# Kernel tuning notes

Measured on AMD Instinct MI355X. Metric: run time of the kernel, lower is better.

## Reference

```python
import jax, jax.numpy as jnp
import numpy as np

EPS = 1e-5

def setup_inputs() -> dict:
    key = jax.random.key(0)
    ks = jax.random.split(key, 10)
    B, S, C, Q, D = 16, 2048, 768, 1024, 64
    clamp3_features = jax.random.normal(ks[0], (B, S, C), dtype=jnp.float32)
    residual = jax.random.normal(ks[1], (B, S, Q), dtype=jnp.float32)
    # params (xavier-ish scale; up-proj given small random values instead of zeros
    # so the output is non-trivial for correctness testing)
    Wproj = jax.random.normal(ks[2], (Q, C), dtype=jnp.float32) * (1.0 / np.sqrt(C))
    Wdown = jax.random.normal(ks[3], (D, Q), dtype=jnp.float32) * (1.0 / np.sqrt(Q))
    gamma = jnp.ones((D,), dtype=jnp.float32)
    beta = jnp.zeros((D,), dtype=jnp.float32)
    Wl1 = jax.random.normal(ks[4], (D, D), dtype=jnp.float32) * (1.0 / np.sqrt(D))
    bl1 = jnp.zeros((D,), dtype=jnp.float32)
    Wl2 = jax.random.normal(ks[5], (D, D), dtype=jnp.float32) * (1.0 / np.sqrt(D))
    bl2 = jnp.zeros((D,), dtype=jnp.float32)
    Wup = jax.random.normal(ks[6], (Q, D), dtype=jnp.float32) * (1.0 / np.sqrt(D))
    return {"clamp3_features": clamp3_features, "residual": residual,
            "Wproj": Wproj, "Wdown": Wdown, "gamma": gamma, "beta": beta,
            "Wl1": Wl1, "bl1": bl1, "Wl2": Wl2, "bl2": bl2, "Wup": Wup}

def _layernorm(x, gamma, beta):
    mu = jnp.mean(x, axis=-1, keepdims=True)
    var = jnp.mean(jnp.square(x - mu), axis=-1, keepdims=True)
    return (x - mu) * jax.lax.rsqrt(var + EPS) * gamma + beta

def reference(clamp3_features, residual, Wproj, Wdown, gamma, beta, Wl1, bl1, Wl2, bl2, Wup):
    # projection (no bias) -> down (no bias) -> LayerNorm
    projected = jnp.einsum('bsc,qc->bsq', clamp3_features, Wproj)
    down = jnp.einsum('bsq,dq->bsd', projected, Wdown)
    normed = _layernorm(down, gamma, beta)
    # SwiGLU: swish(l1(x)) * l2(x)
    o1 = jnp.einsum('bsd,ed->bse', normed, Wl1) + bl1
    swish = o1 * jax.nn.sigmoid(o1)
    gate = jnp.einsum('bsd,ed->bse', normed, Wl2) + bl2
    activated = swish * gate  # dropout is identity in eval mode
    up = jnp.einsum('bsd,qd->bsq', activated, Wup)
    return residual + up
```

## Files before the change

kernel.cpp:

```cpp
#include <hip/hip_runtime.h>


#define CDIM 768
#define QDIM 1024

typedef __attribute__((ext_vector_type(8))) short bf16x8;
typedef __attribute__((ext_vector_type(4))) float f32x4;

__device__ __forceinline__ ushort f2bf(float f) {
  union { float f; unsigned u; } v; v.f = f;
  unsigned r = v.u + 0x7fffu + ((v.u >> 16) & 1u);
  return (ushort)(r >> 16);
}

__global__ void k_wcomb(const float* __restrict__ Wproj, const float* __restrict__ Wdown,
                        float* __restrict__ part) {
  int bid = blockIdx.x;
  int cb = bid % 12, db = (bid / 12) % 8, qc = bid / 96;
  int l = threadIdx.x;
  int c = cb * 64 + l;
  float acc[8];
  #pragma unroll
  for (int i = 0; i < 8; ++i) acc[i] = 0.f;
  int q0 = qc * 128;
  for (int q = q0; q < q0 + 128; ++q) {
    float xp = Wproj[q * CDIM + c];
    #pragma unroll
    for (int i = 0; i < 8; ++i)
      acc[i] = fmaf(Wdown[(db * 8 + i) * QDIM + q], xp, acc[i]);
  }
  #pragma unroll
  for (int i = 0; i < 8; ++i)
    part[((size_t)qc * CDIM + c) * 64 + db * 8 + i] = acc[i];
}

__global__ void k_arrange(const float* __restrict__ part, const float* __restrict__ Wup,
                          const float* __restrict__ Wl1, const float* __restrict__ Wl2,
                          ushort* __restrict__ wcf, ushort* __restrict__ wupf,
                          ushort* __restrict__ wl1f, ushort* __restrict__ wl2f) {
  int idx = blockIdx.x * 256 + threadIdx.x;
  if (idx < 49152) {
    int i0 = idx;
    int j = i0 & 7, l = (i0 >> 3) & 63, t = i0 >> 9;
    int g = l >> 4, r16 = l & 15;
    int nf = t & 3, ks = t >> 2;
    int k = 32 * ks + 8 * g + j, n = 16 * nf + r16;
    float s = 0.f;
    #pragma unroll
    for (int qc = 0; qc < 8; ++qc) s += part[((size_t)qc * CDIM + k) * 64 + n];
    wcf[i0] = f2bf(s);
  } else if (idx < 49152 + 65536) {
    int i2 = idx - 49152;
    int j = i2 & 7, l = (i2 >> 3) & 63, t = i2 >> 9;
    int g = l >> 4, r16 = l & 15;
    int ks = t & 1, nf = t >> 1;
    int k = 32 * ks + 8 * g + j, n = 16 * nf + r16;
    wupf[i2] = f2bf(Wup[n * 64 + k]);
  } else if (idx < 49152 + 65536 + 4096) {
    int i3 = idx - (49152 + 65536);
    int j = i3 & 7, l = (i3 >> 3) & 63, t = i3 >> 9;
    int g = l >> 4, r16 = l & 15;
    int nf = t & 3, ks = t >> 2;
    int k = 32 * ks + 8 * g + j, e = 16 * nf + r16;
    wl1f[i3] = f2bf(Wl1[e * 64 + k]);
  } else {
    int i4 = idx - (49152 + 65536 + 4096);
    int j = i4 & 7, l = (i4 >> 3) & 63, t = i4 >> 9;
    int g = l >> 4, r16 = l & 15;
    int nf = t & 3, ks = t >> 2;
    int k = 32 * ks + 8 * g + j, e = 16 * nf + r16;
    wl2f[i4] = f2bf(Wl2[e * 64 + k]);
  }
}

__global__ __launch_bounds__(256, 6)
void k_act(const float* __restrict__ xg,
           const float* __restrict__ gamma, const float* __restrict__ beta,
           const float* __restrict__ bl1, const float* __restrict__ bl2,
           const ushort* __restrict__ wcf,
           const ushort* __restrict__ wl1f, const ushort* __restrict__ wl2f,
           ushort* __restrict__ ag) {
  __shared__ ushort smem[12416];
  ushort (*x_lds)[776] = reinterpret_cast<ushort(*)[776]>(smem);
  float  (*d_lds)[68]  = reinterpret_cast<float (*)[68]>(smem);
  ushort (*n_lds)[72]  = reinterpret_cast<ushort(*)[72]>(reinterpret_cast<char*>(smem) + 4608);
  ushort (*a_lds)[72]  = reinterpret_cast<ushort(*)[72]>(reinterpret_cast<char*>(smem) + 8192);

  const int tid = threadIdx.x;
  const int w = tid >> 6, l = tid & 63, g = l >> 4, r16 = l & 15;
  const int row0 = blockIdx.x * 16;

  #pragma unroll
  for (int i = 0; i < 12; ++i) {
    int f4 = i * 256 + tid;
    int r = f4 / 192;
    int c4 = (f4 - r * 192) * 4;
    const float4 v = *reinterpret_cast<const float4*>(xg + (size_t)(row0 + r) * CDIM + c4);
    ushort4 b;
    b.x = f2bf(v.x); b.y = f2bf(v.y); b.z = f2bf(v.z); b.w = f2bf(v.w);
    *reinterpret_cast<ushort4*>(&x_lds[r][c4]) = b;
  }
  __syncthreads();

  f32x4 dacc = {0.f, 0.f, 0.f, 0.f};
  #pragma unroll 8
  for (int ks = 0; ks < 24; ++ks) {
    bf16x8 a = *reinterpret_cast<const bf16x8*>(&x_lds[r16][ks * 32 + 8 * g]);
    bf16x8 b = *reinterpret_cast<const bf16x8*>(wcf + ((size_t)(ks * 4 + w) * 64 + l) * 8);
    dacc = __builtin_amdgcn_mfma_f32_16x16x32_bf16(a, b, dacc, 0, 0, 0);
  }
  __syncthreads();
  #pragma unroll
  for (int rg = 0; rg < 4; ++rg) d_lds[4 * g + rg][16 * w + r16] = dacc[rg];
  __syncthreads();

  {
    int row = 4 * w + g;
    f32x4 v = *reinterpret_cast<const f32x4*>(&d_lds[row][4 * r16]);
    float s  = v[0] + v[1] + v[2] + v[3];
    float sq = v[0]*v[0] + v[1]*v[1] + v[2]*v[2] + v[3]*v[3];
    #pragma unroll
    for (int m = 1; m < 16; m <<= 1) {
      s  += __shfl_xor(s, m, 64);
      sq += __shfl_xor(sq, m, 64);
    }
    float mu  = s * (1.f / 64.f);
    float var = sq * (1.f / 64.f) - mu * mu;
    float rs  = rsqrtf(var + 1e-5f);
    const float4 gm = *reinterpret_cast<const float4*>(gamma + 4 * r16);
    const float4 bt = *reinterpret_cast<const float4*>(beta  + 4 * r16);
    ushort4 nb;
    nb.x = f2bf((v[0] - mu) * rs * gm.x + bt.x);
    nb.y = f2bf((v[1] - mu) * rs * gm.y + bt.y);
    nb.z = f2bf((v[2] - mu) * rs * gm.z + bt.z);
    nb.w = f2bf((v[3] - mu) * rs * gm.w + bt.w);
    *reinterpret_cast<ushort4*>(&n_lds[row][4 * r16]) = nb;
  }
  __syncthreads();

  {
    bf16x8 a0 = *reinterpret_cast<const bf16x8*>(&n_lds[r16][8 * g]);
    bf16x8 a1 = *reinterpret_cast<const bf16x8*>(&n_lds[r16][32 + 8 * g]);
    bf16x8 b10 = *reinterpret_cast<const bf16x8*>(wl1f + ((size_t)(0 * 4 + w) * 64 + l) * 8);
    bf16x8 b11 = *reinterpret_cast<const bf16x8*>(wl1f + ((size_t)(1 * 4 + w) * 64 + l) * 8);
    bf16x8 b20 = *reinterpret_cast<const bf16x8*>(wl2f + ((size_t)(0 * 4 + w) * 64 + l) * 8);
    bf16x8 b21 = *reinterpret_cast<const bf16x8*>(wl2f + ((size_t)(1 * 4 + w) * 64 + l) * 8);
    f32x4 z = {0.f, 0.f, 0.f, 0.f};
    f32x4 acc1 = __builtin_amdgcn_mfma_f32_16x16x32_bf16(a0, b10, z, 0, 0, 0);
    acc1 = __builtin_amdgcn_mfma_f32_16x16x32_bf16(a1, b11, acc1, 0, 0, 0);
    f32x4 acc2 = __builtin_amdgcn_mfma_f32_16x16x32_bf16(a0, b20, z, 0, 0, 0);
    acc2 = __builtin_amdgcn_mfma_f32_16x16x32_bf16(a1, b21, acc2, 0, 0, 0);
    float bv1 = bl1[16 * w + r16];
    float bv2 = bl2[16 * w + r16];
    #pragma unroll
    for (int rg = 0; rg < 4; ++rg) {
      float o1 = acc1[rg] + bv1;
      float o2 = acc2[rg] + bv2;
      float sw = o1 / (1.f + __expf(-o1));
      a_lds[4 * g + rg][16 * w + r16] = f2bf(sw * o2);
    }
  }
  __syncthreads();

  if (tid < 128) {
    int r = tid >> 3, c = 8 * (tid & 7);
    bf16x8 v = *reinterpret_cast<const bf16x8*>(&a_lds[r][c]);
    *reinterpret_cast<bf16x8*>(ag + (size_t)(row0 + r) * 64 + c) = v;
  }
}

__global__ __launch_bounds__(256, 3)
void k_up(const ushort* __restrict__ ag, const float* __restrict__ resg,
          const ushort* __restrict__ wupf, float* __restrict__ outg) {
  __shared__ float  bounce[16][512];
  __shared__ ushort a_lds[16][68];
  const int tid = threadIdx.x;
  const int w = tid >> 6, l = tid & 63, g = l >> 4, r16 = l & 15;
  const int row0 = blockIdx.x * 16;

  {
    int e = tid * 4;
    int r = e >> 6, c = e & 63;
    ushort4 v = *reinterpret_cast<const ushort4*>(ag + (size_t)(row0 + r) * 64 + c);
    *reinterpret_cast<ushort4*>(&a_lds[r][c]) = v;
  }
  __syncthreads();
  const bf16x8 af0 = *reinterpret_cast<const bf16x8*>(&a_lds[r16][8 * g]);
  const bf16x8 af1 = *reinterpret_cast<const bf16x8*>(&a_lds[r16][32 + 8 * g]);

  #pragma unroll
  for (int p = 0; p < 2; ++p) {
    f32x4 acc[8];
    #pragma unroll
    for (int i = 0; i < 8; ++i) {
      size_t nf = 32 * p + 8 * w + i;
      bf16x8 b0 = *reinterpret_cast<const bf16x8*>(wupf + ((nf * 2 + 0) * 64 + l) * 8);
      bf16x8 b1 = *reinterpret_cast<const bf16x8*>(wupf + ((nf * 2 + 1) * 64 + l) * 8);
      f32x4 t = {0.f, 0.f, 0.f, 0.f};
      t = __builtin_amdgcn_mfma_f32_16x16x32_bf16(b0, af0, t, 0, 0, 0);
      acc[i] = __builtin_amdgcn_mfma_f32_16x16x32_bf16(b1, af1, t, 0, 0, 0);
    }
    if (p) __syncthreads();
    #pragma unroll
    for (int i = 0; i < 8; ++i) {
      int q = 32 * w + 4 * i + g;
      *reinterpret_cast<f32x4*>(&bounce[r16][4 * (q ^ (r16 & 7))]) = acc[i];
    }
    __syncthreads();
    #pragma unroll
    for (int s = 0; s < 8; ++s) {
      int row = 2 * s + (tid >> 7);
      int cq  = tid & 127;
      size_t goff = (size_t)(row0 + row) * QDIM + 512 * p + 4 * cq;
      f32x4 rv = *reinterpret_cast<const f32x4*>(resg + goff);
      f32x4 bv = *reinterpret_cast<const f32x4*>(&bounce[row][4 * (cq ^ (row & 7))]);
      *reinterpret_cast<f32x4*>(outg + goff) = rv + bv;
    }
  }
}

extern "C" void kernel_launch(void* const* d_in, const int* in_sizes, int n_in,
                              void* d_out, int out_size, void* d_ws, size_t ws_size,
                              hipStream_t stream) {
  (void)in_sizes; (void)n_in; (void)out_size; (void)ws_size;
  const float* x     = (const float*)d_in[0];
  const float* resid = (const float*)d_in[1];
  const float* Wproj = (const float*)d_in[2];
  const float* Wdown = (const float*)d_in[3];
  const float* gamma = (const float*)d_in[4];
  const float* beta  = (const float*)d_in[5];
  const float* Wl1   = (const float*)d_in[6];
  const float* bl1   = (const float*)d_in[7];
  const float* Wl2   = (const float*)d_in[8];
  const float* bl2   = (const float*)d_in[9];
  const float* Wup   = (const float*)d_in[10];
  float* out = (float*)d_out;

  char* ws = (char*)d_ws;
  float*  part = (float*)(ws);
  ushort* wcf  = (ushort*)(ws + 1572864);
  ushort* wupf = (ushort*)(ws + 1671168);
  ushort* wl1f = (ushort*)(ws + 1802240);
  ushort* wl2f = (ushort*)(ws + 1810432);
  ushort* ag   = (ushort*)(ws + 1818624);

  k_wcomb  <<<768, 64, 0, stream>>>(Wproj, Wdown, part);
  k_arrange<<<480, 256, 0, stream>>>(part, Wup, Wl1, Wl2, wcf, wupf, wl1f, wl2f);
  k_act    <<<2048, 256, 0, stream>>>(x, gamma, beta, bl1, bl2, wcf, wl1f, wl2f, ag);
  k_up     <<<2048, 256, 0, stream>>>(ag, resid, wupf, out);
}
```

Before: 126.1 us.

## Stream activations and residual via async global-to-LDS loads with pipelined ring

k_act now copies fp32 input rows straight into swizzled LDS with global_load_lds and converts to bf16 at fragment-load time, which doubles LDS use and lowers the occupancy hint. k_up computes all 64 output fragments in one pass, stores the up-projection as bf16 in a swizzled bounce buffer, and streams residual rows through a 4-slot LDS ring using async loads with manual vmcnt waits. The aim is to overlap the residual reads with compute and cut register and LDS pressure. The trade-offs are lower occupancy in k_act, and rounding the up-projection to bf16 before the residual add adds precision error.

```diff
diff --git a/kernel.cpp b/kernel.cpp
--- a/kernel.cpp
+++ b/kernel.cpp
@@ -1,4 +1,5 @@
 #include <hip/hip_runtime.h>
+#include <hip/hip_bf16.h>
 
 
 #define CDIM 768
@@ -6,11 +7,20 @@
 
 typedef __attribute__((ext_vector_type(8))) short bf16x8;
 typedef __attribute__((ext_vector_type(4))) float f32x4;
+
+#define WAITV(n) asm volatile("s_waitcnt vmcnt(" #n ")" ::: "memory")
+#define SCHED0() __builtin_amdgcn_sched_barrier(0)
 
 __device__ __forceinline__ ushort f2bf(float f) {
   union { float f; unsigned u; } v; v.f = f;
   unsigned r = v.u + 0x7fffu + ((v.u >> 16) & 1u);
   return (ushort)(r >> 16);
+}
+
+__device__ __forceinline__ void gload16(const float* g, float* lds) {
+  __builtin_amdgcn_global_load_lds(
+      (const __attribute__((address_space(1))) void*)g,
+      (__attribute__((address_space(3))) void*)lds, 16, 0, 0);
 }
 
 __global__ void k_wcomb(const float* __restrict__ Wproj, const float* __restrict__ Wdown,
@@ -73,18 +83,18 @@
   }
 }
 
-__global__ __launch_bounds__(256, 6)
+__global__ __launch_bounds__(256, 3)
 void k_act(const float* __restrict__ xg,
            const float* __restrict__ gamma, const float* __restrict__ beta,
            const float* __restrict__ bl1, const float* __restrict__ bl2,
            const ushort* __restrict__ wcf,
            const ushort* __restrict__ wl1f, const ushort* __restrict__ wl2f,
            ushort* __restrict__ ag) {
-  __shared__ ushort smem[12416];
-  ushort (*x_lds)[776] = reinterpret_cast<ushort(*)[776]>(smem);
+  __shared__ alignas(16) ushort smem[24576];
   float  (*d_lds)[68]  = reinterpret_cast<float (*)[68]>(smem);
   ushort (*n_lds)[72]  = reinterpret_cast<ushort(*)[72]>(reinterpret_cast<char*>(smem) + 4608);
   ushort (*a_lds)[72]  = reinterpret_cast<ushort(*)[72]>(reinterpret_cast<char*>(smem) + 8192);
+  float* xf = reinterpret_cast<float*>(smem);
 
   const int tid = threadIdx.x;
   const int w = tid >> 6, l = tid & 63, g = l >> 4, r16 = l & 15;
@@ -93,21 +103,28 @@
   #pragma unroll
   for (int i = 0; i < 12; ++i) {
     int f4 = i * 256 + tid;
-    int r = f4 / 192;
-    int c4 = (f4 - r * 192) * 4;
-    const float4 v = *reinterpret_cast<const float4*>(xg + (size_t)(row0 + r) * CDIM + c4);
-    ushort4 b;
-    b.x = f2bf(v.x); b.y = f2bf(v.y); b.z = f2bf(v.z); b.w = f2bf(v.w);
-    *reinterpret_cast<ushort4*>(&x_lds[r][c4]) = b;
+    int r  = f4 / 192;
+    int u  = f4 - r * 192;
+    const float* src = xg + (size_t)(row0 + r) * CDIM + ((u ^ (r & 7)) << 2);
+    gload16(src, xf + (size_t)(i * 256 + (w << 6)) * 4);
   }
   __syncthreads();
 
   f32x4 dacc = {0.f, 0.f, 0.f, 0.f};
+  const int rx = r16 & 7;
+  const float* rowp = xf + r16 * 768;
   #pragma unroll 8
   for (int ks = 0; ks < 24; ++ks) {
-    bf16x8 a = *reinterpret_cast<const bf16x8*>(&x_lds[r16][ks * 32 + 8 * g]);
+    int u0 = ks * 8 + 2 * g;
+    f32x4 xa = *reinterpret_cast<const f32x4*>(rowp + ((u0 ^ rx) << 2));
+    f32x4 xb = *reinterpret_cast<const f32x4*>(rowp + (((u0 + 1) ^ rx) << 2));
+    union { bf16x8 v; __hip_bfloat16 h[8]; } fa;
+    fa.h[0] = __float2bfloat16(xa[0]); fa.h[1] = __float2bfloat16(xa[1]);
+    fa.h[2] = __float2bfloat16(xa[2]); fa.h[3] = __float2bfloat16(xa[3]);
+    fa.h[4] = __float2bfloat16(xb[0]); fa.h[5] = __float2bfloat16(xb[1]);
+    fa.h[6] = __float2bfloat16(xb[2]); fa.h[7] = __float2bfloat16(xb[3]);
     bf16x8 b = *reinterpret_cast<const bf16x8*>(wcf + ((size_t)(ks * 4 + w) * 64 + l) * 8);
-    dacc = __builtin_amdgcn_mfma_f32_16x16x32_bf16(a, b, dacc, 0, 0, 0);
+    dacc = __builtin_amdgcn_mfma_f32_16x16x32_bf16(fa.v, b, dacc, 0, 0, 0);
   }
   __syncthreads();
   #pragma unroll
@@ -172,8 +189,9 @@
 __global__ __launch_bounds__(256, 3)
 void k_up(const ushort* __restrict__ ag, const float* __restrict__ resg,
           const ushort* __restrict__ wupf, float* __restrict__ outg) {
-  __shared__ float  bounce[16][512];
-  __shared__ ushort a_lds[16][68];
+  __shared__ alignas(16) ushort a_lds[16][68];
+  __shared__ alignas(16) ushort bounce[16][1024];
+  __shared__ alignas(16) float  ring[4][1024];
   const int tid = threadIdx.x;
   const int w = tid >> 6, l = tid & 63, g = l >> 4, r16 = l & 15;
   const int row0 = blockIdx.x * 16;
@@ -184,38 +202,61 @@
     ushort4 v = *reinterpret_cast<const ushort4*>(ag + (size_t)(row0 + r) * 64 + c);
     *reinterpret_cast<ushort4*>(&a_lds[r][c]) = v;
   }
-  __syncthreads();
-  const bf16x8 af0 = *reinterpret_cast<const bf16x8*>(&a_lds[r16][8 * g]);
-  const bf16x8 af1 = *reinterpret_cast<const bf16x8*>(&a_lds[r16][32 + 8 * g]);
-
-  #pragma unroll
-  for (int p = 0; p < 2; ++p) {
-    f32x4 acc[8];
-    #pragma unroll
-    for (int i = 0; i < 8; ++i) {
-      size_t nf = 32 * p + 8 * w + i;
+  asm volatile("s_waitcnt lgkmcnt(0)" ::: "memory");
+  __builtin_amdgcn_s_barrier();
+  SCHED0();
+
+  #pragma unroll
+  for (int s = 0; s < 3; ++s)
+    gload16(resg + (size_t)(row0 + s) * QDIM + 4 * tid, &ring[s][w << 8]);
+  SCHED0();
+
+  {
+    const bf16x8 af0 = *reinterpret_cast<const bf16x8*>(&a_lds[r16][8 * g]);
+    const bf16x8 af1 = *reinterpret_cast<const bf16x8*>(&a_lds[r16][32 + 8 * g]);
+    #pragma unroll
+    for (int i = 0; i < 16; ++i) {
+      size_t nf = 16 * w + i;
       bf16x8 b0 = *reinterpret_cast<const bf16x8*>(wupf + ((nf * 2 + 0) * 64 + l) * 8);
       bf16x8 b1 = *reinterpret_cast<const bf16x8*>(wupf + ((nf * 2 + 1) * 64 + l) * 8);
       f32x4 t = {0.f, 0.f, 0.f, 0.f};
       t = __builtin_amdgcn_mfma_f32_16x16x32_bf16(b0, af0, t, 0, 0, 0);
-      acc[i] = __builtin_amdgcn_mfma_f32_16x16x32_bf16(b1, af1, t, 0, 0, 0);
+      t = __builtin_amdgcn_mfma_f32_16x16x32_bf16(b1, af1, t, 0, 0, 0);
+      ushort4 ub;
+      ub.x = f2bf(t[0]); ub.y = f2bf(t[1]); ub.z = f2bf(t[2]); ub.w = f2bf(t[3]);
+      int q = 64 * w + 4 * i + g;
+      int p = q ^ ((r16 & 7) << 2);
+      *reinterpret_cast<ushort4*>(&bounce[r16][p << 2]) = ub;
     }
-    if (p) __syncthreads();
-    #pragma unroll
-    for (int i = 0; i < 8; ++i) {
-      int q = 32 * w + 4 * i + g;
-      *reinterpret_cast<f32x4*>(&bounce[r16][4 * (q ^ (r16 & 7))]) = acc[i];
-    }
-    __syncthreads();
-    #pragma unroll
-    for (int s = 0; s < 8; ++s) {
-      int row = 2 * s + (tid >> 7);
-      int cq  = tid & 127;
-      size_t goff = (size_t)(row0 + row) * QDIM + 512 * p + 4 * cq;
-      f32x4 rv = *reinterpret_cast<const f32x4*>(resg + goff);
-      f32x4 bv = *reinterpret_cast<const f32x4*>(&bounce[row][4 * (cq ^ (row & 7))]);
-      *reinterpret_cast<f32x4*>(outg + goff) = rv + bv;
-    }
+  }
+  asm volatile("s_waitcnt lgkmcnt(0)" ::: "memory");
+  __builtin_amdgcn_s_barrier();
+  SCHED0();
+
+  #pragma unroll
+  for (int s = 0; s < 16; ++s) {
+    SCHED0();
+    if (s < 13)
+      gload16(resg + (size_t)(row0 + s + 3) * QDIM + 4 * tid, &ring[(s + 3) & 3][w << 8]);
+    SCHED0();
+    if      (s == 0)  WAITV(3);
+    else if (s == 1)  WAITV(4);
+    else if (s == 2)  WAITV(5);
+    else if (s <= 12) WAITV(6);
+    else if (s == 13) WAITV(5);
+    else if (s == 14) WAITV(4);
+    else              WAITV(3);
+    SCHED0();
+    f32x4 rv = *reinterpret_cast<const f32x4*>(&ring[s & 3][tid << 2]);
+    int p = tid ^ ((s & 7) << 2);
+    ushort4 ub = *reinterpret_cast<const ushort4*>(&bounce[s][p << 2]);
+    union { float f; unsigned u; } c0, c1, c2, c3;
+    c0.u = (unsigned)ub.x << 16; c1.u = (unsigned)ub.y << 16;
+    c2.u = (unsigned)ub.z << 16; c3.u = (unsigned)ub.w << 16;
+    f32x4 o;
+    o[0] = rv[0] + c0.f; o[1] = rv[1] + c1.f;
+    o[2] = rv[2] + c2.f; o[3] = rv[3] + c3.f;
+    *reinterpret_cast<f32x4*>(outg + (size_t)(row0 + s) * QDIM + 4 * tid) = o;
   }
 }
 
```

After: 130.7 us. +3.6%, slower.
